# Optimization experiments

Hardware: AMD Instinct MI355X
Metric: run time of the kernel (lower is better)

Reference implementation:

```python
import jax, jax.numpy as jnp
import numpy as np
from jax import lax

B, J, C, K, TOK, CH, H = 2048, 17, 480, 3, 64, 960, 6
HD = C // H  # 80
EPS = 1e-5

def gelu(x):
    return jax.nn.gelu(x, approximate=False)

def layernorm(x, g, b):
    mu = jnp.mean(x, axis=-1, keepdims=True)
    var = jnp.var(x, axis=-1, keepdims=True)
    return (x - mu) * lax.rsqrt(var + EPS) * g + b

def groupnorm(x, g, b, groups=16):
    # x: (B, C, J) -> normalize over (C//groups * J) per group
    n, c, j = x.shape
    xg = x.reshape(n, groups, -1)
    mu = jnp.mean(xg, axis=-1, keepdims=True)
    var = jnp.var(xg, axis=-1, keepdims=True)
    xg = (xg - mu) * lax.rsqrt(var + EPS)
    return xg.reshape(n, c, j) * g[None, :, None] + b[None, :, None]

def dwconv1d(x, w, b, pad):
    # x: (B, C, J), w: (C, 1, Kw) depthwise
    y = lax.conv_general_dilated(x, w, window_strides=(1,), padding=[(pad, pad)],
                                 dimension_numbers=('NCH', 'OIH', 'NCH'),
                                 feature_group_count=x.shape[1])
    return y + b[None, :, None]

def setup_inputs() -> dict:
    key = jax.random.key(0)
    ks = jax.random.split(key, 16)
    n = jax.random.normal
    return {
        'x': n(ks[0], (B, J, C), dtype=jnp.float32),
        'adj': n(ks[1], (K, J, J), dtype=jnp.float32) * 0.1,
        'norm1_g': jnp.ones((J,), jnp.float32), 'norm1_b': jnp.zeros((J,), jnp.float32),
        'gcn1_w': n(ks[2], (C * K, C), jnp.float32) * 0.02, 'gcn1_b': jnp.zeros((C * K,), jnp.float32),
        'dw_w': n(ks[3], (C, 1, 7), jnp.float32) * 0.1, 'dw_b': jnp.zeros((C,), jnp.float32),
        'dwgn_g': jnp.ones((C,), jnp.float32), 'dwgn_b': jnp.zeros((C,), jnp.float32),
        'mlp1_w1': n(ks[4], (TOK, J), jnp.float32) * 0.02, 'mlp1_b1': jnp.zeros((TOK,), jnp.float32),
        'mlp1_w2': n(ks[5], (J, TOK), jnp.float32) * 0.02, 'mlp1_b2': jnp.zeros((J,), jnp.float32),
        'qkv_w': n(ks[6], (3 * C, C), jnp.float32) * 0.02, 'qkv_b': jnp.zeros((3 * C,), jnp.float32),
        'proj_w': n(ks[7], (C, C), jnp.float32) * 0.02, 'proj_b': jnp.zeros((C,), jnp.float32),
        'pos_w': n(ks[8], (C, 1, 9), jnp.float32) * 0.1, 'pos_b': jnp.zeros((C,), jnp.float32),
        'gnf_g': jnp.ones((C,), jnp.float32), 'gnf_b': jnp.zeros((C,), jnp.float32),
        'norm2_g': jnp.ones((C,), jnp.float32), 'norm2_b': jnp.zeros((C,), jnp.float32),
        'gcn2_w': n(ks[9], (C * K, C), jnp.float32) * 0.02, 'gcn2_b': jnp.zeros((C * K,), jnp.float32),
        'mlp2_w1': n(ks[10], (CH, C), jnp.float32) * 0.02, 'mlp2_b1': jnp.zeros((CH,), jnp.float32),
        'mlp2_w2': n(ks[11], (C, CH), jnp.float32) * 0.02, 'mlp2_b2': jnp.zeros((C,), jnp.float32),
    }

def reference(x, adj, norm1_g, norm1_b, gcn1_w, gcn1_b, dw_w, dw_b, dwgn_g, dwgn_b,
              mlp1_w1, mlp1_b1, mlp1_w2, mlp1_b2, qkv_w, qkv_b, proj_w, proj_b,
              pos_w, pos_b, gnf_g, gnf_b, norm2_g, norm2_b, gcn2_w, gcn2_b,
              mlp2_w1, mlp2_b1, mlp2_w2, mlp2_b2):
    b = x.shape[0]
    xc = jnp.transpose(x, (0, 2, 1))            # (b, c, j)
    res_spatial = xc
    xn = layernorm(xc, norm1_g, norm1_b)        # LN over joints
    # --- GCN branch 1: 1x1 conv then adjacency einsum ---
    y = jnp.einsum('bcj,oc->boj', xn, gcn1_w) + gcn1_b[None, :, None]
    y = y.reshape(b, K, C, J)
    x_gcn1 = jnp.einsum('bkcv,kvw->bcw', y, adj)  # (b, c, j)
    # --- depthwise conv + GN + GELU + token Mlp ---
    d = gelu(groupnorm(dwconv1d(xn, dw_w, dw_b, 3), dwgn_g, dwgn_b))
    x_mjem = gelu(d @ mlp1_w1.T + mlp1_b1) @ mlp1_w2.T + mlp1_b2  # mix over j
    # --- spatial global attention (6 heads over joints + dwconv pos) ---
    xt = jnp.transpose(xn, (0, 2, 1))           # (b, j, c)
    qkv = xt @ qkv_w.T + qkv_b                  # (b, j, 3c)
    qkv = qkv.reshape(b, J, 3, H, HD).transpose(2, 0, 3, 1, 4)  # (3, b, h, j, hd)
    q, k, v = qkv[0], qkv[1], qkv[2]
    attn = jax.nn.softmax(jnp.einsum('bhqd,bhkd->bhqk', q, k) * (HD ** -0.5), axis=-1)
    o = jnp.einsum('bhqk,bhkd->bhqd', attn, v).transpose(0, 2, 1, 3).reshape(b, J, C)
    o = o @ proj_w.T + proj_b
    x_gsa = jnp.transpose(o, (0, 2, 1)) + dwconv1d(xn, pos_w, pos_b, 4)  # (b, c, j)
    # --- fuse ---
    fused = groupnorm(x_gsa + x_gcn1 + x_mjem, gnf_g, gnf_b)
    xc = res_spatial + gelu(fused)
    # --- channel stage ---
    xj = jnp.transpose(xc, (0, 2, 1))           # (b, j, c)
    res_channel = xj
    xn2 = layernorm(xj, norm2_g, norm2_b)       # LN over channels
    xcc = jnp.transpose(xn2, (0, 2, 1))         # (b, c, j)
    y2 = jnp.einsum('bcj,oc->boj', xcc, gcn2_w) + gcn2_b[None, :, None]
    y2 = y2.reshape(b, K, C, J)
    x_gcn2 = jnp.transpose(jnp.einsum('bkcv,kvw->bcw', y2, adj), (0, 2, 1))  # (b, j, c)
    mlp_out = gelu(xn2 @ mlp2_w1.T + mlp2_b1) @ mlp2_w2.T + mlp2_b2
    # sca_block is undefined in the source __init__ -> identity
    return res_channel + mlp_out + x_gcn2
```

## Files before the change

### kernel.cpp

```cpp
#include <hip/hip_runtime.h>
#include <hip/hip_bf16.h>

#define DI __device__ __forceinline__

typedef __attribute__((ext_vector_type(8))) short bf16x8;
typedef __attribute__((ext_vector_type(4))) float f32x4;

namespace {
constexpr int B_ = 2048, J_ = 17, C_ = 480, K_ = 3, TOK_ = 64, CH_ = 960, H_ = 6, HD_ = 80;
constexpr int C3_ = 3 * C_;
constexpr float EPSF = 1e-5f;
}

DI float gelu_f(float x) { return 0.5f * x * (1.0f + erff(x * 0.70710678118654752f)); }
DI float b2f(__hip_bfloat16 v) { return __bfloat162float(v); }
DI __hip_bfloat16 f2b(float v) { return __float2bfloat16(v); }
DI float s2f(short s) { return __uint_as_float(((unsigned)(unsigned short)s) << 16); }

DI void gl16(const void* g, void* l) {
  __builtin_amdgcn_global_load_lds(
      (const __attribute__((address_space(1))) unsigned int*)g,
      (__attribute__((address_space(3))) unsigned int*)l, 16, 0, 0);
}

__global__ __launch_bounds__(256) void cvt_kernel(const float* __restrict__ s,
                                                  __hip_bfloat16* __restrict__ d, int n) {
  int i = blockIdx.x * 256 + threadIdx.x;
  if (i < n) d[i] = f2b(s[i]);
}

__global__ __launch_bounds__(256) void ln1_kernel(const float* __restrict__ x,
                                                  const float* __restrict__ g,
                                                  const float* __restrict__ bt,
                                                  __hip_bfloat16* __restrict__ xnT, int nBC) {
  const int t = blockIdx.x * 256 + threadIdx.x;
  if (t >= nBC) return;
  const int b = t / C_, c = t % C_;
  const float* xp = x + (size_t)b * J_ * C_ + c;
  float v[J_];
  float s = 0.f;
  #pragma unroll
  for (int j = 0; j < J_; ++j) { v[j] = xp[j * C_]; s += v[j]; }
  const float mu = s * (1.f / J_);
  float sq = 0.f;
  #pragma unroll
  for (int j = 0; j < J_; ++j) { const float d = v[j] - mu; sq += d * d; }
  const float rs = rsqrtf(sq * (1.f / J_) + EPSF);
  __hip_bfloat16* op = xnT + (size_t)b * J_ * C_ + c;
  #pragma unroll
  for (int j = 0; j < J_; ++j) op[j * C_] = f2b((v[j] - mu) * rs * g[j] + bt[j]);
}

template<int KD, int EPI>
__global__ __launch_bounds__(256) void gemm_lds(const __hip_bfloat16* __restrict__ A,
                                                const __hip_bfloat16* __restrict__ W,
                                                const float* __restrict__ bias,
                                                __hip_bfloat16* __restrict__ Dst, int Ntot,
                                                const __hip_bfloat16* __restrict__ r1,
                                                const __hip_bfloat16* __restrict__ r2,
                                                float* __restrict__ outf) {
  constexpr int NST = (KD + 63) / 64;
  constexpr bool TAIL = (KD % 64) != 0;
  constexpr int ROWB = KD * 2;
  __shared__ __align__(16) char smem[57344];

  const int lane = threadIdx.x & 63;
  const int wid  = threadIdx.x >> 6;
  const int m0g = blockIdx.x * 128;
  const int n0g = blockIdx.y * 96;

  const int srow = lane >> 3;
  const int scbs = ((lane & 7) * 16) ^ ((srow & 7) << 4);
  auto stage = [&](int t, int bi) {
    const int kb = t * 128;
    const int ab = bi * 16384;
    const int bb = 32768 + bi * 12288;
    #pragma unroll
    for (int i = wid; i < 16; i += 4) {
      const int r = i * 8 + srow;
      gl16((const char*)A + (size_t)(m0g + r) * ROWB + kb + scbs, smem + ab + i * 1024);
    }
    #pragma unroll
    for (int i = wid; i < 12; i += 4) {
      const int r = i * 8 + srow;
      gl16((const char*)W + (size_t)(n0g + r) * ROWB + kb + scbs, smem + bb + i * 1024);
    }
  };

  const f32x4 zf = {0.f, 0.f, 0.f, 0.f};
  f32x4 acc[4][3];
  #pragma unroll
  for (int mi = 0; mi < 4; ++mi)
    #pragma unroll
    for (int ni = 0; ni < 3; ++ni) acc[mi][ni] = zf;

  const int rA0 = (wid >> 1) * 64 + (lane & 15);
  const int rB0 = (wid & 1) * 48 + (lane & 15);
  const int swz = (lane & 7) << 4;
  const int kq  = (lane >> 4) * 16;

  stage(0, 0);
  __syncthreads();
  int buf = 0;
  for (int t = 0; t < NST; ++t) {
    if (t + 1 < NST) stage(t + 1, buf ^ 1);
    const int abase = buf * 16384;
    const int bbase = 32768 + buf * 12288;
    const int nks = (TAIL && t == NST - 1) ? 1 : 2;
    for (int ks = 0; ks < nks; ++ks) {
      const int cb = (ks * 64 + kq) ^ swz;
      bf16x8 av[4], bv[3];
      #pragma unroll
      for (int mi = 0; mi < 4; ++mi)
        av[mi] = *reinterpret_cast<const bf16x8*>(smem + abase + (rA0 + mi * 16) * 128 + cb);
      #pragma unroll
      for (int ni = 0; ni < 3; ++ni)
        bv[ni] = *reinterpret_cast<const bf16x8*>(smem + bbase + (rB0 + ni * 16) * 128 + cb);
      #pragma unroll
      for (int mi = 0; mi < 4; ++mi)
        #pragma unroll
        for (int ni = 0; ni < 3; ++ni)
          acc[mi][ni] = __builtin_amdgcn_mfma_f32_16x16x32_bf16(av[mi], bv[ni], acc[mi][ni], 0, 0, 0);
    }
    __syncthreads();
    buf ^= 1;
  }

  const int col0 = n0g + (wid & 1) * 48 + (lane & 15);
  const int r0   = m0g + (wid >> 1) * 64 + ((lane >> 4) << 2);
  #pragma unroll
  for (int ni = 0; ni < 3; ++ni) {
    const int col = col0 + ni * 16;
    const float bvv = bias[col];
    #pragma unroll
    for (int mi = 0; mi < 4; ++mi) {
      #pragma unroll
      for (int r = 0; r < 4; ++r) {
        const size_t idx = (size_t)(r0 + mi * 16 + r) * Ntot + col;
        float v = acc[mi][ni][r] + bvv;
        if (EPI == 1) v = gelu_f(v);
        if (EPI == 2) outf[idx] = v + b2f(r1[idx]) + b2f(r2[idx]);
        else Dst[idx] = f2b(v);
      }
    }
  }
}

__global__ __launch_bounds__(256) void attn_kernel(const __hip_bfloat16* __restrict__ qkv,
                                                   __hip_bfloat16* __restrict__ o) {
  const int b = blockIdx.x, tid = threadIdx.x;
  __shared__ __hip_bfloat16 sqkv[J_][C3_];
  __shared__ float S[H_][J_][J_];
  {
    const uint4* src = (const uint4*)(qkv + (size_t)b * J_ * C3_);
    uint4* dst = (uint4*)&sqkv[0][0];
    for (int i = tid; i < 3060; i += 256) dst[i] = src[i];
  }
  __syncthreads();
  for (int i = tid; i < H_ * J_ * J_; i += 256) {
    const int h = i / (J_ * J_), r = i % (J_ * J_), qj = r / J_, kj = r % J_;
    const bf16x8* qp = (const bf16x8*)&sqkv[qj][h * HD_];
    const bf16x8* kp = (const bf16x8*)&sqkv[kj][C_ + h * HD_];
    float acc = 0.f;
    #pragma unroll
    for (int d8 = 0; d8 < HD_ / 8; ++d8) {
      const bf16x8 qv = qp[d8], kv = kp[d8];
      #pragma unroll
      for (int t = 0; t < 8; ++t) acc += s2f(qv[t]) * s2f(kv[t]);
    }
    S[h][qj][kj] = acc * 0.11180339887498949f;
  }
  __syncthreads();
  if (tid < H_ * J_) {
    const int h = tid / J_, qj = tid % J_;
    float* row = S[h][qj];
    float m = row[0];
    #pragma unroll
    for (int kk = 1; kk < J_; ++kk) m = fmaxf(m, row[kk]);
    float s = 0.f;
    #pragma unroll
    for (int kk = 0; kk < J_; ++kk) { const float e = __expf(row[kk] - m); row[kk] = e; s += e; }
    const float inv = 1.f / s;
    #pragma unroll
    for (int kk = 0; kk < J_; ++kk) row[kk] *= inv;
  }
  __syncthreads();
  __hip_bfloat16* ob = o + (size_t)b * J_ * C_;
  for (int i = tid; i < J_ * C_; i += 256) {
    const int qj = i / C_, c = i % C_;
    const int h = c / HD_;
    const float* srow = S[h][qj];
    float acc = 0.f;
    #pragma unroll
    for (int kk = 0; kk < J_; ++kk) acc += srow[kk] * b2f(sqkv[kk][2 * C_ + c]);
    ob[i] = f2b(acc);
  }
}

__global__ __launch_bounds__(512) void gcn_contract_kernel(const __hip_bfloat16* __restrict__ y,
                                                           const float* __restrict__ adj,
                                                           __hip_bfloat16* __restrict__ g) {
  const int b = blockIdx.x, tid = threadIdx.x;
  __shared__ float adjl[K_ * J_ * J_];
  for (int i = tid; i < K_ * J_ * J_; i += 512) adjl[i] = adj[i];
  __syncthreads();
  const int c = tid;
  if (c < C_) {
    float yv[K_][J_];
    const __hip_bfloat16* yb = y + (size_t)b * J_ * C3_ + c;
    #pragma unroll
    for (int k = 0; k < K_; ++k)
      #pragma unroll
      for (int v = 0; v < J_; ++v)
        yv[k][v] = b2f(yb[(size_t)v * C3_ + k * C_]);
    __hip_bfloat16* gp = g + (size_t)b * J_ * C_ + c;
    #pragma unroll
    for (int w = 0; w < J_; ++w) {
      float acc = 0.f;
      #pragma unroll
      for (int k = 0; k < K_; ++k)
        #pragma unroll
        for (int v = 0; v < J_; ++v)
          acc += yv[k][v] * adjl[(k * J_ + v) * J_ + w];
      gp[w * C_] = f2b(acc);
    }
  }
}

__global__ __launch_bounds__(512) void dwmlp_kernel(const __hip_bfloat16* __restrict__ xnT,
    const float* __restrict__ dww, const float* __restrict__ dwb,
    const float* __restrict__ gg, const float* __restrict__ gb,
    const float* __restrict__ w1, const float* __restrict__ b1,
    const float* __restrict__ w2, const float* __restrict__ b2,
    __hip_bfloat16* __restrict__ mjem) {
  const int b = blockIdx.x, tid = threadIdx.x;
  __shared__ float xl[J_][C_];
  __shared__ float gstat[16][2];
  __shared__ float w1l[TOK_ * J_], w2l[J_ * TOK_], b1l[TOK_], b2l[J_];
  const __hip_bfloat16* src = xnT + (size_t)b * J_ * C_;
  for (int i = tid; i < J_ * C_; i += 512) ((float*)xl)[i] = b2f(src[i]);
  for (int i = tid; i < TOK_ * J_; i += 512) w1l[i] = w1[i];
  for (int i = tid; i < J_ * TOK_; i += 512) w2l[i] = w2[i];
  if (tid < TOK_) b1l[tid] = b1[tid];
  if (tid < J_) b2l[tid] = b2[tid];
  if (tid < 32) gstat[tid >> 1][tid & 1] = 0.f;
  __syncthreads();
  const int c = tid;
  float dv[J_];
  if (c < C_) {
    float wv[7];
    #pragma unroll
    for (int t = 0; t < 7; ++t) wv[t] = dww[c * 7 + t];
    const float bias = dwb[c];
    float s = 0.f, sqs = 0.f;
    #pragma unroll
    for (int j = 0; j < J_; ++j) {
      float acc = bias;
      #pragma unroll
      for (int t = 0; t < 7; ++t) {
        const int jj = j - 3 + t;
        if (jj >= 0 && jj < J_) acc += xl[jj][c] * wv[t];
      }
      dv[j] = acc; s += acc; sqs += acc * acc;
    }
    atomicAdd(&gstat[c / 30][0], s);
    atomicAdd(&gstat[c / 30][1], sqs);
  }
  __syncthreads();
  if (c < C_) {
    const float mu = gstat[c / 30][0] * (1.f / 510.f);
    const float var = gstat[c / 30][1] * (1.f / 510.f) - mu * mu;
    const float rs = rsqrtf(var + EPSF);
    const float sc = gg[c], of = gb[c];
    #pragma unroll
    for (int j = 0; j < J_; ++j) dv[j] = gelu_f((dv[j] - mu) * rs * sc + of);
    float mj[J_];
    #pragma unroll
    for (int j = 0; j < J_; ++j) mj[j] = b2l[j];
    for (int t = 0; t < TOK_; ++t) {
      float acc = b1l[t];
      #pragma unroll
      for (int j = 0; j < J_; ++j) acc += dv[j] * w1l[t * J_ + j];
      const float hg = gelu_f(acc);
      #pragma unroll
      for (int j = 0; j < J_; ++j) mj[j] += hg * w2l[j * TOK_ + t];
    }
    __hip_bfloat16* dst = mjem + (size_t)b * J_ * C_ + c;
    #pragma unroll
    for (int j = 0; j < J_; ++j) dst[j * C_] = f2b(mj[j]);
  }
}

__global__ __launch_bounds__(512) void fuse_kernel(
    const float* __restrict__ x, const __hip_bfloat16* __restrict__ xnT,
    const __hip_bfloat16* __restrict__ g1o, const __hip_bfloat16* __restrict__ projo,
    const __hip_bfloat16* __restrict__ mjem,
    const float* __restrict__ posw, const float* __restrict__ posb,
    const float* __restrict__ gnfg, const float* __restrict__ gnfb,
    const float* __restrict__ n2g, const float* __restrict__ n2b,
    __hip_bfloat16* __restrict__ resch, __hip_bfloat16* __restrict__ xn2) {
  const int b = blockIdx.x, tid = threadIdx.x;
  __shared__ float xcl[J_][C_];
  __shared__ float gstat[16][2];
  __shared__ float lnst[J_][2];
  if (tid < 32) gstat[tid >> 1][tid & 1] = 0.f;
  __syncthreads();
  const int c = tid;
  float fz[J_];
  if (c < C_) {
    float xnv[J_];
    const __hip_bfloat16* xp = xnT + (size_t)b * J_ * C_ + c;
    #pragma unroll
    for (int j = 0; j < J_; ++j) xnv[j] = b2f(xp[j * C_]);
    float pw[9];
    #pragma unroll
    for (int t = 0; t < 9; ++t) pw[t] = posw[c * 9 + t];
    const float pb = posb[c];
    const __hip_bfloat16* pj = projo + (size_t)b * J_ * C_ + c;
    const __hip_bfloat16* mp = mjem + (size_t)b * J_ * C_ + c;
    const __hip_bfloat16* gp = g1o + (size_t)b * J_ * C_ + c;
    float s = 0.f, sqs = 0.f;
    #pragma unroll
    for (int j = 0; j < J_; ++j) {
      float pos = pb;
      #pragma unroll
      for (int t = 0; t < 9; ++t) {
        const int jj = j - 4 + t;
        if (jj >= 0 && jj < J_) pos += xnv[jj] * pw[t];
      }
      const float f = b2f(pj[j * C_]) + pos + b2f(gp[j * C_]) + b2f(mp[j * C_]);
      fz[j] = f; s += f; sqs += f * f;
    }
    atomicAdd(&gstat[c / 30][0], s);
    atomicAdd(&gstat[c / 30][1], sqs);
  }
  __syncthreads();
  if (c < C_) {
    const float mu = gstat[c / 30][0] * (1.f / 510.f);
    const float var = gstat[c / 30][1] * (1.f / 510.f) - mu * mu;
    const float rs = rsqrtf(var + EPSF);
    const float sc = gnfg[c], of = gnfb[c];
    const float* xr = x + (size_t)b * J_ * C_ + c;
    __hip_bfloat16* rp = resch + (size_t)b * J_ * C_ + c;
    #pragma unroll
    for (int j = 0; j < J_; ++j) {
      const float xcv = xr[j * C_] + gelu_f((fz[j] - mu) * rs * sc + of);
      xcl[j][c] = xcv;
      rp[j * C_] = f2b(xcv);
    }
  }
  __syncthreads();
  const int wid = tid >> 6, lane = tid & 63;
  for (int j = wid; j < J_; j += 8) {
    float ls = 0.f, lq = 0.f;
    for (int cc = lane; cc < C_; cc += 64) { const float v = xcl[j][cc]; ls += v; lq += v * v; }
    #pragma unroll
    for (int off = 32; off > 0; off >>= 1) { ls += __shfl_xor(ls, off); lq += __shfl_xor(lq, off); }
    if (lane == 0) {
      const float mu = ls * (1.f / C_);
      const float var = lq * (1.f / C_) - mu * mu;
      lnst[j][0] = mu; lnst[j][1] = rsqrtf(var + EPSF);
    }
  }
  __syncthreads();
  if (c < C_) {
    const float sc = n2g[c], of = n2b[c];
    __hip_bfloat16* xp2 = xn2 + (size_t)b * J_ * C_ + c;
    #pragma unroll
    for (int j = 0; j < J_; ++j)
      xp2[j * C_] = f2b((xcl[j][c] - lnst[j][0]) * lnst[j][1] * sc + of);
  }
}

extern "C" void kernel_launch(void* const* d_in, const int* in_sizes, int n_in,
                              void* d_out, int out_size, void* d_ws, size_t ws_size,
                              hipStream_t stream) {
  const float* x      = (const float*)d_in[0];
  const float* adj    = (const float*)d_in[1];
  const float* n1g    = (const float*)d_in[2];
  const float* n1b    = (const float*)d_in[3];
  const float* gcn1_w = (const float*)d_in[4];
  const float* gcn1_b = (const float*)d_in[5];
  const float* dw_w   = (const float*)d_in[6];
  const float* dw_b   = (const float*)d_in[7];
  const float* dwgn_g = (const float*)d_in[8];
  const float* dwgn_b = (const float*)d_in[9];
  const float* m1w1   = (const float*)d_in[10];
  const float* m1b1   = (const float*)d_in[11];
  const float* m1w2   = (const float*)d_in[12];
  const float* m1b2   = (const float*)d_in[13];
  const float* qkv_w  = (const float*)d_in[14];
  const float* qkv_b  = (const float*)d_in[15];
  const float* proj_w = (const float*)d_in[16];
  const float* proj_b = (const float*)d_in[17];
  const float* pos_w  = (const float*)d_in[18];
  const float* pos_b  = (const float*)d_in[19];
  const float* gnf_g  = (const float*)d_in[20];
  const float* gnf_b  = (const float*)d_in[21];
  const float* n2g    = (const float*)d_in[22];
  const float* n2b    = (const float*)d_in[23];
  const float* gcn2_w = (const float*)d_in[24];
  const float* gcn2_b = (const float*)d_in[25];
  const float* m2w1   = (const float*)d_in[26];
  const float* m2b1   = (const float*)d_in[27];
  const float* m2w2   = (const float*)d_in[28];
  const float* m2b2   = (const float*)d_in[29];
  float* out = (float*)d_out;
  char* ws = (char*)d_ws;
  (void)in_sizes; (void)n_in; (void)out_size;

  auto a256 = [](size_t b) { return (b + 255) & ~(size_t)255; };
  const size_t wbytes = 3 * a256((size_t)C3_ * C_ * 2) + a256((size_t)C_ * C_ * 2) +
                        a256((size_t)CH_ * C_ * 2) + a256((size_t)C_ * CH_ * 2);
  int nch = 16;
  for (int cand : {1, 2, 4, 8, 16}) {
    const size_t Mcb = (size_t)(B_ / cand) * J_;
    const size_t fp = wbytes + a256(Mcb * C3_ * 2) + 6 * a256(Mcb * C_ * 2);
    if (fp <= ws_size) { nch = cand; break; }
  }
  const int Bc = B_ / nch;
  const int Mc = Bc * J_;

  size_t off = 0;
  auto alloc = [&](size_t bytes) { char* p = ws + off; off += a256(bytes); return p; };
  __hip_bfloat16* w_qkv = (__hip_bfloat16*)alloc((size_t)C3_ * C_ * 2);
  __hip_bfloat16* w_g1  = (__hip_bfloat16*)alloc((size_t)C3_ * C_ * 2);
  __hip_bfloat16* w_g2  = (__hip_bfloat16*)alloc((size_t)C3_ * C_ * 2);
  __hip_bfloat16* w_pr  = (__hip_bfloat16*)alloc((size_t)C_ * C_ * 2);
  __hip_bfloat16* w_21  = (__hip_bfloat16*)alloc((size_t)CH_ * C_ * 2);
  __hip_bfloat16* w_22  = (__hip_bfloat16*)alloc((size_t)C_ * CH_ * 2);
  __hip_bfloat16* BIG   = (__hip_bfloat16*)alloc((size_t)Mc * C3_ * 2);
  __hip_bfloat16* xnT   = (__hip_bfloat16*)alloc((size_t)Mc * C_ * 2);
  __hip_bfloat16* attno = (__hip_bfloat16*)alloc((size_t)Mc * C_ * 2);
  __hip_bfloat16* projo = (__hip_bfloat16*)alloc((size_t)Mc * C_ * 2);
  __hip_bfloat16* mjem  = (__hip_bfloat16*)alloc((size_t)Mc * C_ * 2);
  __hip_bfloat16* g1o   = (__hip_bfloat16*)alloc((size_t)Mc * C_ * 2);
  __hip_bfloat16* resch = (__hip_bfloat16*)alloc((size_t)Mc * C_ * 2);
  __hip_bfloat16* xn2   = attno;
  __hip_bfloat16* g2o   = g1o;
  __hip_bfloat16* hbuf  = BIG;

  auto cvt = [&](const float* s, __hip_bfloat16* d, int n) {
    cvt_kernel<<<(n + 255) / 256, 256, 0, stream>>>(s, d, n);
  };
  cvt(qkv_w,  w_qkv, C3_ * C_);
  cvt(gcn1_w, w_g1,  C3_ * C_);
  cvt(gcn2_w, w_g2,  C3_ * C_);
  cvt(proj_w, w_pr,  C_ * C_);
  cvt(m2w1,   w_21,  CH_ * C_);
  cvt(m2w2,   w_22,  C_ * CH_);

  for (int ci = 0; ci < nch; ++ci) {
    const float* xc = x + (size_t)ci * Bc * J_ * C_;
    float* outc = out + (size_t)ci * Bc * J_ * C_;
    ln1_kernel<<<(Bc * C_ + 255) / 256, 256, 0, stream>>>(xc, n1g, n1b, xnT, Bc * C_);
    gemm_lds<C_, 0><<<dim3(Mc / 128, C3_ / 96), 256, 0, stream>>>(xnT, w_qkv, qkv_b, BIG, C3_, nullptr, nullptr, nullptr);
    attn_kernel<<<Bc, 256, 0, stream>>>(BIG, attno);
    gemm_lds<C_, 0><<<dim3(Mc / 128, C3_ / 96), 256, 0, stream>>>(xnT, w_g1, gcn1_b, BIG, C3_, nullptr, nullptr, nullptr);
    gcn_contract_kernel<<<Bc, 512, 0, stream>>>(BIG, adj, g1o);
    gemm_lds<C_, 0><<<dim3(Mc / 128, C_ / 96), 256, 0, stream>>>(attno, w_pr, proj_b, projo, C_, nullptr, nullptr, nullptr);
    dwmlp_kernel<<<Bc, 512, 0, stream>>>(xnT, dw_w, dw_b, dwgn_g, dwgn_b, m1w1, m1b1, m1w2, m1b2, mjem);
    fuse_kernel<<<Bc, 512, 0, stream>>>(xc, xnT, g1o, projo, mjem, pos_w, pos_b,
                                        gnf_g, gnf_b, n2g, n2b, resch, xn2);
    gemm_lds<C_, 0><<<dim3(Mc / 128, C3_ / 96), 256, 0, stream>>>(xn2, w_g2, gcn2_b, BIG, C3_, nullptr, nullptr, nullptr);
    gcn_contract_kernel<<<Bc, 512, 0, stream>>>(BIG, adj, g2o);
    gemm_lds<C_, 1><<<dim3(Mc / 128, CH_ / 96), 256, 0, stream>>>(xn2, w_21, m2b1, hbuf, CH_, nullptr, nullptr, nullptr);
    gemm_lds<CH_, 2><<<dim3(Mc / 128, C_ / 96), 256, 0, stream>>>(hbuf, w_22, m2b2, nullptr, C_, resch, g2o, outc);
  }
}
```

Before: 857.9 us.

## Merge weight conversions into one vectorized kernel and restructure dwmlp token MLP

Replaces the six per-weight fp32-to-bf16 conversion launches with a single kernel that converts four elements per thread into the contiguous weight workspace. In dwmlp, the input tile stays in LDS as bf16 and is copied with 16-byte loads instead of being widened to fp32. The token-MLP weights now come straight from global memory rather than LDS, and the loop is reordered so all 64 hidden values are computed first in registers with FMAs, then projected back. The fully unrolled 64-entry array raises register pressure at 512 threads per block and may cut occupancy. The single-kernel conversion assumes the weight buffers are allocated contiguously in this order.

```diff
diff --git a/kernel.cpp b/kernel.cpp
--- a/kernel.cpp
+++ b/kernel.cpp
@@ -23,10 +23,27 @@
       (__attribute__((address_space(3))) unsigned int*)l, 16, 0, 0);
 }
 
-__global__ __launch_bounds__(256) void cvt_kernel(const float* __restrict__ s,
-                                                  __hip_bfloat16* __restrict__ d, int n) {
-  int i = blockIdx.x * 256 + threadIdx.x;
-  if (i < n) d[i] = f2b(s[i]);
+__global__ __launch_bounds__(256) void cvt_all_kernel(
+    const float* __restrict__ s0, const float* __restrict__ s1,
+    const float* __restrict__ s2, const float* __restrict__ s3,
+    const float* __restrict__ s4, const float* __restrict__ s5,
+    __hip_bfloat16* __restrict__ d) {
+  constexpr int SG = C3_ * C_;
+  constexpr int O1 = SG, O2 = 2 * SG, O3 = 3 * SG;
+  constexpr int O4 = O3 + C_ * C_;
+  constexpr int O5 = O4 + CH_ * C_;
+  const int i = (blockIdx.x * 256 + threadIdx.x) * 4;
+  const float* s; int off;
+  if      (i < O1) { s = s0; off = i; }
+  else if (i < O2) { s = s1; off = i - O1; }
+  else if (i < O3) { s = s2; off = i - O2; }
+  else if (i < O4) { s = s3; off = i - O3; }
+  else if (i < O5) { s = s4; off = i - O4; }
+  else             { s = s5; off = i - O5; }
+  const float4 v = *reinterpret_cast<const float4*>(s + off);
+  union { ushort4 u; __hip_bfloat16 h[4]; } o;
+  o.h[0] = f2b(v.x); o.h[1] = f2b(v.y); o.h[2] = f2b(v.z); o.h[3] = f2b(v.w);
+  *reinterpret_cast<ushort4*>(reinterpret_cast<unsigned short*>(d) + i) = o.u;
 }
 
 __global__ __launch_bounds__(256) void ln1_kernel(const float* __restrict__ x,
@@ -234,15 +251,13 @@
     const float* __restrict__ w2, const float* __restrict__ b2,
     __hip_bfloat16* __restrict__ mjem) {
   const int b = blockIdx.x, tid = threadIdx.x;
-  __shared__ float xl[J_][C_];
+  __shared__ __hip_bfloat16 xl[J_][C_];
   __shared__ float gstat[16][2];
-  __shared__ float w1l[TOK_ * J_], w2l[J_ * TOK_], b1l[TOK_], b2l[J_];
-  const __hip_bfloat16* src = xnT + (size_t)b * J_ * C_;
-  for (int i = tid; i < J_ * C_; i += 512) ((float*)xl)[i] = b2f(src[i]);
-  for (int i = tid; i < TOK_ * J_; i += 512) w1l[i] = w1[i];
-  for (int i = tid; i < J_ * TOK_; i += 512) w2l[i] = w2[i];
-  if (tid < TOK_) b1l[tid] = b1[tid];
-  if (tid < J_) b2l[tid] = b2[tid];
+  {
+    const uint4* src = (const uint4*)(xnT + (size_t)b * J_ * C_);
+    uint4* dst = (uint4*)&xl[0][0];
+    for (int i = tid; i < 1020; i += 512) dst[i] = src[i];
+  }
   if (tid < 32) gstat[tid >> 1][tid & 1] = 0.f;
   __syncthreads();
   const int c = tid;
@@ -259,7 +274,7 @@
       #pragma unroll
       for (int t = 0; t < 7; ++t) {
         const int jj = j - 3 + t;
-        if (jj >= 0 && jj < J_) acc += xl[jj][c] * wv[t];
+        if (jj >= 0 && jj < J_) acc += b2f(xl[jj][c]) * wv[t];
       }
       dv[j] = acc; s += acc; sqs += acc * acc;
     }
@@ -274,16 +289,25 @@
     const float sc = gg[c], of = gb[c];
     #pragma unroll
     for (int j = 0; j < J_; ++j) dv[j] = gelu_f((dv[j] - mu) * rs * sc + of);
+    float h[TOK_];
+    #pragma unroll
+    for (int t = 0; t < TOK_; ++t) h[t] = b1[t];
+    #pragma unroll
+    for (int j = 0; j < J_; ++j) {
+      const float d = dv[j];
+      #pragma unroll
+      for (int t = 0; t < TOK_; ++t) h[t] = fmaf(d, w1[t * J_ + j], h[t]);
+    }
+    #pragma unroll
+    for (int t = 0; t < TOK_; ++t) h[t] = gelu_f(h[t]);
     float mj[J_];
     #pragma unroll
-    for (int j = 0; j < J_; ++j) mj[j] = b2l[j];
+    for (int j = 0; j < J_; ++j) mj[j] = b2[j];
+    #pragma unroll
     for (int t = 0; t < TOK_; ++t) {
-      float acc = b1l[t];
-      #pragma unroll
-      for (int j = 0; j < J_; ++j) acc += dv[j] * w1l[t * J_ + j];
-      const float hg = gelu_f(acc);
-      #pragma unroll
-      for (int j = 0; j < J_; ++j) mj[j] += hg * w2l[j * TOK_ + t];
+      const float hg = h[t];
+      #pragma unroll
+      for (int j = 0; j < J_; ++j) mj[j] = fmaf(hg, w2[j * TOK_ + t], mj[j]);
     }
     __hip_bfloat16* dst = mjem + (size_t)b * J_ * C_ + c;
     #pragma unroll
@@ -440,15 +464,7 @@
   __hip_bfloat16* g2o   = g1o;
   __hip_bfloat16* hbuf  = BIG;
 
-  auto cvt = [&](const float* s, __hip_bfloat16* d, int n) {
-    cvt_kernel<<<(n + 255) / 256, 256, 0, stream>>>(s, d, n);
-  };
-  cvt(qkv_w,  w_qkv, C3_ * C_);
-  cvt(gcn1_w, w_g1,  C3_ * C_);
-  cvt(gcn2_w, w_g2,  C3_ * C_);
-  cvt(proj_w, w_pr,  C_ * C_);
-  cvt(m2w1,   w_21,  CH_ * C_);
-  cvt(m2w2,   w_22,  C_ * CH_);
+  cvt_all_kernel<<<3150, 256, 0, stream>>>(qkv_w, gcn1_w, gcn2_w, proj_w, m2w1, m2w2, w_qkv);
 
   for (int ci = 0; ci < nch; ++ci) {
     const float* xc = x + (size_t)ci * Bc * J_ * C_;
```

Result: faster. 835.8 us (-2.6%).
